# Kernel optimization log

Hardware: AMD Instinct MI355X
Metric: run time of the kernel (lower is better)

Reference implementation:

```python
import jax, jax.numpy as jnp
import numpy as np

B, D, S = 16384, 1024, 2048
LN_EPS = 1e-5


def setup_inputs() -> dict:
    key = jax.random.key(0)
    ks = jax.random.split(key, 16)
    inv_d = 1.0 / np.sqrt(D)
    inv_s = 1.0 / np.sqrt(S)
    inv_ds = 1.0 / np.sqrt(D + S)
    return {
        "x_t": jax.random.normal(ks[0], (B, D), jnp.float32),
        "state": jax.random.normal(ks[1], (B, S), jnp.float32),
        "conditioning": jax.random.normal(ks[2], (B, D), jnp.float32),
        "carry_scale": jax.random.uniform(ks[3], (B, S), jnp.float32),
        # Linear weights stored [in, out] (y = x @ W + b); equivalent math to torch's x @ W.T
        "W_step": jax.random.normal(ks[4], (D, S), jnp.float32) * inv_d,
        "b_step": jnp.zeros((S,), jnp.float32),
        "W_cstep": jax.random.normal(ks[5], (D, S), jnp.float32) * inv_d,
        "W_in": jax.random.normal(ks[6], (D, S), jnp.float32) * inv_d,
        "b_in": jnp.zeros((S,), jnp.float32),
        "W_cin": jax.random.normal(ks[7], (D, S), jnp.float32) * inv_d,
        "W_state": jax.random.normal(ks[8], (S, S), jnp.float32) * inv_s,
        "W_out": jax.random.normal(ks[9], (D + S, D), jnp.float32) * inv_ds,
        "b_out": jnp.zeros((D,), jnp.float32),
        "ln_w": jnp.ones((D,), jnp.float32),
        "ln_b": jnp.zeros((D,), jnp.float32),
        "log_decay": jnp.zeros((S,), jnp.float32),
    }


def reference(x_t, state, conditioning, carry_scale,
              W_step, b_step, W_cstep, W_in, b_in, W_cin,
              W_state, W_out, b_out, ln_w, ln_b, log_decay):
    # input-conditioned step size
    step = jax.nn.softplus(x_t @ W_step + b_step)
    step = step + 0.1 * jax.nn.softplus(conditioning @ W_cstep)
    # candidate state
    proposal = jnp.tanh(x_t @ W_in + b_in + conditioning @ W_cin + state @ W_state)
    # diagonal decay gate
    decay = jnp.exp(-step * jnp.exp(log_decay)) * carry_scale
    new_state = decay * state + (1.0 - decay) * proposal
    # output projection + residual LayerNorm
    out = jnp.concatenate([x_t, new_state], axis=-1) @ W_out + b_out
    h = out + x_t
    mu = jnp.mean(h, axis=-1, keepdims=True)
    var = jnp.mean(jnp.square(h - mu), axis=-1, keepdims=True)
    output = (h - mu) * jax.lax.rsqrt(var + LN_EPS) * ln_w + ln_b
    return output, new_state
```

## Files before the change

kernel.cpp:

```cpp
#include <hip/hip_runtime.h>
#include <hip/hip_bf16.h>
#include <cstdint>
#include <cstddef>

#define BB 16384
#define DD 1024
#define SS 2048

typedef __attribute__((ext_vector_type(8))) short s8vec;
typedef __attribute__((ext_vector_type(4))) short s4vec;
typedef __attribute__((ext_vector_type(4))) float f4vec;

static __device__ __forceinline__ short f2bf(float x) {
  __hip_bfloat16 h = __float2bfloat16(x);
  union { __hip_bfloat16 b; short s; } u; u.b = h; return u.s;
}

static __device__ __forceinline__ float softplus_f(float x) {
  return (x > 20.f) ? x : log1pf(expf(x));
}

static __device__ __forceinline__ void gload16(const void* g, void* l) {
  __builtin_amdgcn_global_load_lds((__attribute__((address_space(1))) void*)g,
                                   (__attribute__((address_space(3))) void*)l,
                                   16, 0, 0);
}

struct EpiParams {
  float* out;
  const float* bias;
  const float* step;
  const float* state;
  const float* carry;
  const float* ldec;
  float* out_state;
  short* xy;
  const float* x;
};

#define BAR() do { asm volatile("" ::: "memory"); __builtin_amdgcn_s_barrier(); asm volatile("" ::: "memory"); } while (0)
#define WAIT_LGKM0() do { asm volatile("s_waitcnt lgkmcnt(0)" ::: "memory"); __builtin_amdgcn_sched_barrier(0); } while (0)
#define WAIT_VM(n)   do { asm volatile("s_waitcnt vmcnt(" #n ")" ::: "memory"); __builtin_amdgcn_sched_barrier(0); } while (0)

template<int EPI>
__global__ __launch_bounds__(512, 2)
void gemm256(const short* __restrict__ A, int lda,
             const short* __restrict__ Bt, int ldb,
             int K, int nbxl, EpiParams ep)
{
  __shared__ short lds0[65536];

  const int tid  = threadIdx.x;
  const int lane = tid & 63;
  const int w    = tid >> 6;
  const int wm   = w >> 2;
  const int wn   = w & 3;
  const int frow = lane & 15;
  const int klane = lane >> 4;
  const int swb  = lane & 7;

  const int lin = blockIdx.x;
  const int bm  = lin >> nbxl;
  const int bn  = lin & ((1 << nbxl) - 1);

  const int rl0    = w * 16 + (lane >> 3);
  const int colsw8 = ((lane & 7) ^ ((lane >> 3) & 7)) * 8;
  const int dOff   = w * 1024 + lane * 8;

  const short* gA0 = A  + (size_t)(bm * 256 +       rl0) * lda + colsw8;
  const short* gA1 = A  + (size_t)(bm * 256 + 128 + rl0) * lda + colsw8;
  const short* gB0 = Bt + (size_t)(bn * 256 +       rl0) * ldb + colsw8;
  const short* gB1 = Bt + (size_t)(bn * 256 + 128 + rl0) * ldb + colsw8;
  const int kmax = K - 64;

  auto STAGE = [&](int buf, int h, int kt) {
    const short* g = (h == 0) ? gA0 : (h == 1) ? gA1 : (h == 2) ? gB0 : gB1;
    const int ld = (h < 2) ? lda : ldb;
    int kk = kt * 64; if (kk > kmax) kk = kmax;
    short* d = &lds0[buf * 32768 + h * 8192 + dOff];
    gload16(g + kk,                 d);
    gload16(g + kk + (size_t)8 * ld, d + 512);
  };

  auto LDA2 = [&](int buf, int frp, s8vec (&a)[2][2]) {
    const short* base = &lds0[buf * 32768 + wm * 8192];
#pragma unroll
    for (int i = 0; i < 2; i++) {
      const int row = (frp * 2 + i) * 16 + frow;
#pragma unroll
      for (int ks = 0; ks < 2; ks++) {
        const int slot = (ks * 4 + klane) ^ swb;
        a[i][ks] = *(const s8vec*)&base[row * 64 + slot * 8];
      }
    }
  };

  auto LDB8 = [&](int buf, s8vec (&b)[4][2]) {
    const short* base = &lds0[buf * 32768 + 16384 + (wn >> 1) * 8192];
#pragma unroll
    for (int fc = 0; fc < 4; fc++) {
      const int row = (wn & 1) * 64 + fc * 16 + frow;
#pragma unroll
      for (int ks = 0; ks < 2; ks++) {
        const int slot = (ks * 4 + klane) ^ swb;
        b[fc][ks] = *(const s8vec*)&base[row * 64 + slot * 8];
      }
    }
  };

  f4vec acc[8][4];
#pragma unroll
  for (int i = 0; i < 8; i++)
#pragma unroll
    for (int j = 0; j < 4; j++) acc[i][j] = (f4vec){0.f, 0.f, 0.f, 0.f};

  s8vec aX[2][2], aY[2][2], bf0[4][2], bf1[4][2];

#define QMFMA(aS, bS, q) do {                                                  \
  _Pragma("unroll") for (int i = 0; i < 2; i++)                                \
  _Pragma("unroll") for (int fc = 0; fc < 4; fc++)                             \
  _Pragma("unroll") for (int ks = 0; ks < 2; ks++)                             \
    acc[(q) * 2 + i][fc] = __builtin_amdgcn_mfma_f32_16x16x32_bf16(            \
        aS[i][ks], bS[fc][ks], acc[(q) * 2 + i][fc], 0, 0, 0);                 \
} while (0)

  STAGE(0, 0, 0); STAGE(0, 1, 0); STAGE(0, 2, 0); STAGE(0, 3, 0);
  STAGE(1, 0, 1);
  WAIT_VM(2);
  BAR();
  LDB8(0, bf0);
  LDA2(0, 0, aX);

  const int J = K >> 7;
  for (int j = 0; j < J; ++j) {
    const int t1 = 2 * j + 1, t2 = 2 * j + 2, t3 = 2 * j + 3;
    LDA2(0, 1, aY); STAGE(1, 1, t1);
    BAR(); WAIT_LGKM0();
    __builtin_amdgcn_s_setprio(1); QMFMA(aX, bf0, 0); __builtin_amdgcn_s_setprio(0);
    BAR();
    LDA2(0, 2, aX); STAGE(1, 2, t1);
    BAR(); WAIT_LGKM0();
    __builtin_amdgcn_s_setprio(1); QMFMA(aY, bf0, 1); __builtin_amdgcn_s_setprio(0);
    BAR();
    LDA2(0, 3, aY); STAGE(1, 3, t1);
    BAR(); WAIT_LGKM0();
    __builtin_amdgcn_s_setprio(1); QMFMA(aX, bf0, 2); __builtin_amdgcn_s_setprio(0);
    BAR();
    STAGE(0, 0, t2);
    WAIT_VM(2);
    BAR();
    LDB8(1, bf1); LDA2(1, 0, aX);
    __builtin_amdgcn_s_setprio(1); QMFMA(aY, bf0, 3); __builtin_amdgcn_s_setprio(0);
    BAR();
    LDA2(1, 1, aY); STAGE(0, 1, t2);
    BAR(); WAIT_LGKM0();
    __builtin_amdgcn_s_setprio(1); QMFMA(aX, bf1, 0); __builtin_amdgcn_s_setprio(0);
    BAR();
    LDA2(1, 2, aX); STAGE(0, 2, t2);
    BAR(); WAIT_LGKM0();
    __builtin_amdgcn_s_setprio(1); QMFMA(aY, bf1, 1); __builtin_amdgcn_s_setprio(0);
    BAR();
    LDA2(1, 3, aY); STAGE(0, 3, t2);
    BAR(); WAIT_LGKM0();
    __builtin_amdgcn_s_setprio(1); QMFMA(aX, bf1, 2); __builtin_amdgcn_s_setprio(0);
    BAR();
    STAGE(1, 0, t3);
    WAIT_VM(2);
    BAR();
    LDB8(0, bf0); LDA2(0, 0, aX);
    __builtin_amdgcn_s_setprio(1); QMFMA(aY, bf1, 3); __builtin_amdgcn_s_setprio(0);
    BAR();
  }
  asm volatile("s_waitcnt vmcnt(0) lgkmcnt(0)" ::: "memory");

  const int r0 = bm * 256 + wm * 128 + (lane >> 4) * 4;
  const int c0 = bn * 256 + wn * 64 + (lane & 15);

#pragma unroll
  for (int fr = 0; fr < 8; fr++) {
#pragma unroll
    for (int fc = 0; fc < 4; fc++) {
      const int col = c0 + fc * 16;
#pragma unroll
      for (int r = 0; r < 4; r++) {
        const int row = r0 + fr * 16 + r;
        const float v = acc[fr][fc][r];
        if constexpr (EPI == 0) {
          ep.out[(size_t)row * SS + col] = softplus_f(v + ep.bias[col]);
        } else if constexpr (EPI == 1) {
          const size_t idx = (size_t)row * SS + col;
          ep.out[idx] = ep.out[idx] + 0.1f * softplus_f(v);
        } else if constexpr (EPI == 2) {
          const size_t idx = (size_t)row * SS + col;
          const float step = ep.step[idx];
          const float dec  = expf(-step * expf(ep.ldec[col])) * ep.carry[idx];
          const float prop = tanhf(v + ep.bias[col]);
          const float ns   = dec * ep.state[idx] + (1.f - dec) * prop;
          ep.out_state[idx] = ns;
          ep.xy[(size_t)row * 3072 + 1024 + col] = f2bf(ns);
        } else {
          const size_t idx = (size_t)row * DD + col;
          ep.out[idx] = v + ep.bias[col] + ep.x[idx];
        }
      }
    }
  }
#undef QMFMA
}

__global__ __launch_bounds__(256)
void tcast(const float* __restrict__ src, int R, int C,
           short* __restrict__ dst, int ldd, int co)
{
  __shared__ float tile[32][33];
  const int c0 = blockIdx.x * 32;
  const int r0 = blockIdx.y * 32;
  const int tx = threadIdx.x;
  const int ty = threadIdx.y;
#pragma unroll
  for (int i = 0; i < 4; i++)
    tile[ty * 4 + i][tx] = src[(size_t)(r0 + ty * 4 + i) * C + c0 + tx];
  __syncthreads();
#pragma unroll
  for (int i = 0; i < 4; i++)
    dst[(size_t)(c0 + ty * 4 + i) * ldd + co + r0 + tx] = f2bf(tile[tx][ty * 4 + i]);
}

__global__ __launch_bounds__(256)
void cast_xc(const float4* __restrict__ x, const float4* __restrict__ c,
             short* __restrict__ Xcat, short* __restrict__ XY)
{
  const size_t i = (size_t)blockIdx.x * 256 + threadIdx.x;
  if (i >= (size_t)BB * (DD / 4)) return;
  const size_t row = i >> 8;
  const int col4 = (int)(i & 255);
  const float4 xv = x[i];
  const float4 cv = c[i];
  const s4vec xs = { f2bf(xv.x), f2bf(xv.y), f2bf(xv.z), f2bf(xv.w) };
  const s4vec cs = { f2bf(cv.x), f2bf(cv.y), f2bf(cv.z), f2bf(cv.w) };
  *(s4vec*)&Xcat[row * 4096 + col4 * 4]        = xs;
  *(s4vec*)&Xcat[row * 4096 + 1024 + col4 * 4] = cs;
  *(s4vec*)&XY[row * 3072 + col4 * 4]          = xs;
}

__global__ __launch_bounds__(256)
void cast_state(const float4* __restrict__ s, short* __restrict__ Xcat)
{
  const size_t i = (size_t)blockIdx.x * 256 + threadIdx.x;
  if (i >= (size_t)BB * (SS / 4)) return;
  const size_t row = i >> 9;
  const int col4 = (int)(i & 511);
  const float4 sv = s[i];
  const s4vec ss = { f2bf(sv.x), f2bf(sv.y), f2bf(sv.z), f2bf(sv.w) };
  *(s4vec*)&Xcat[row * 4096 + 2048 + col4 * 4] = ss;
}

__global__ __launch_bounds__(256)
void ln_kernel(const float* __restrict__ h, const float* __restrict__ w,
               const float* __restrict__ b, float* __restrict__ out)
{
  const int row = blockIdx.x;
  const int t = threadIdx.x;
  const float4 v = ((const float4*)(h + (size_t)row * DD))[t];
  float s  = v.x + v.y + v.z + v.w;
  float sq = v.x * v.x + v.y * v.y + v.z * v.z + v.w * v.w;
#pragma unroll
  for (int off = 32; off; off >>= 1) {
    s  += __shfl_down(s, off);
    sq += __shfl_down(sq, off);
  }
  __shared__ float ss[4], ssq[4];
  const int lane = t & 63, wv = t >> 6;
  if (lane == 0) { ss[wv] = s; ssq[wv] = sq; }
  __syncthreads();
  const float st  = ss[0] + ss[1] + ss[2] + ss[3];
  const float sqt = ssq[0] + ssq[1] + ssq[2] + ssq[3];
  const float mu  = st * (1.f / (float)DD);
  const float var = sqt * (1.f / (float)DD) - mu * mu;
  const float rstd = rsqrtf(var + 1e-5f);
  const float4 wv4 = ((const float4*)w)[t];
  const float4 bv4 = ((const float4*)b)[t];
  float4 o;
  o.x = (v.x - mu) * rstd * wv4.x + bv4.x;
  o.y = (v.y - mu) * rstd * wv4.y + bv4.y;
  o.z = (v.z - mu) * rstd * wv4.z + bv4.z;
  o.w = (v.w - mu) * rstd * wv4.w + bv4.w;
  ((float4*)(out + (size_t)row * DD))[t] = o;
}

extern "C" void kernel_launch(void* const* d_in, const int* in_sizes, int n_in,
                              void* d_out, int out_size, void* d_ws, size_t ws_size,
                              hipStream_t stream)
{
  const float* x_t    = (const float*)d_in[0];
  const float* state  = (const float*)d_in[1];
  const float* cond   = (const float*)d_in[2];
  const float* carry  = (const float*)d_in[3];
  const float* W_step = (const float*)d_in[4];
  const float* b_step = (const float*)d_in[5];
  const float* W_cstep= (const float*)d_in[6];
  const float* W_in   = (const float*)d_in[7];
  const float* b_in   = (const float*)d_in[8];
  const float* W_cin  = (const float*)d_in[9];
  const float* W_state= (const float*)d_in[10];
  const float* W_out  = (const float*)d_in[11];
  const float* b_out  = (const float*)d_in[12];
  const float* ln_w   = (const float*)d_in[13];
  const float* ln_b   = (const float*)d_in[14];
  const float* ldec   = (const float*)d_in[15];

  char* ws = (char*)d_ws;
  size_t off = 0;
  short* Xcat = (short*)(ws + off); off += (size_t)BB * 4096 * 2;
  short* XY   = (short*)(ws + off); off += (size_t)BB * 3072 * 2;
  float* A1   = (float*)(ws + off); off += (size_t)BB * SS * 4;
  short* WstepT  = (short*)(ws + off); off += (size_t)SS * DD * 2;
  short* WcstepT = (short*)(ws + off); off += (size_t)SS * DD * 2;
  short* WcatT   = (short*)(ws + off); off += (size_t)SS * 4096 * 2;
  short* WoutT   = (short*)(ws + off); off += (size_t)DD * 3072 * 2;
  float* hbuf = A1;

  float* out_ln    = (float*)d_out;
  float* out_state = (float*)d_out + (size_t)BB * DD;

  cast_xc<<<dim3(BB * (DD / 4) / 256), 256, 0, stream>>>(
      (const float4*)x_t, (const float4*)cond, Xcat, XY);
  cast_state<<<dim3(BB * (SS / 4) / 256), 256, 0, stream>>>(
      (const float4*)state, Xcat);

  tcast<<<dim3(SS / 32, DD / 32), dim3(32, 8), 0, stream>>>(W_step, DD, SS, WstepT, DD, 0);
  tcast<<<dim3(SS / 32, DD / 32), dim3(32, 8), 0, stream>>>(W_cstep, DD, SS, WcstepT, DD, 0);
  tcast<<<dim3(SS / 32, DD / 32), dim3(32, 8), 0, stream>>>(W_in,   DD, SS, WcatT, 4096, 0);
  tcast<<<dim3(SS / 32, DD / 32), dim3(32, 8), 0, stream>>>(W_cin,  DD, SS, WcatT, 4096, 1024);
  tcast<<<dim3(SS / 32, SS / 32), dim3(32, 8), 0, stream>>>(W_state, SS, SS, WcatT, 4096, 2048);
  tcast<<<dim3(DD / 32, 3072 / 32), dim3(32, 8), 0, stream>>>(W_out, 3072, DD, WoutT, 3072, 0);

  const int nwgS = (BB / 256) * (SS / 256);
  const int nwgD = (BB / 256) * (DD / 256);

  EpiParams p1{}; p1.out = A1; p1.bias = b_step;
  gemm256<0><<<dim3(nwgS), 512, 0, stream>>>(Xcat, 4096, WstepT, DD, 1024, 3, p1);

  EpiParams p2{}; p2.out = A1;
  gemm256<1><<<dim3(nwgS), 512, 0, stream>>>(Xcat + 1024, 4096, WcstepT, DD, 1024, 3, p2);

  EpiParams p3{};
  p3.bias = b_in; p3.step = A1; p3.state = state; p3.carry = carry;
  p3.ldec = ldec; p3.out_state = out_state; p3.xy = XY;
  gemm256<2><<<dim3(nwgS), 512, 0, stream>>>(Xcat, 4096, WcatT, 4096, 4096, 3, p3);

  EpiParams p4{}; p4.out = hbuf; p4.bias = b_out; p4.x = x_t;
  gemm256<3><<<dim3(nwgD), 512, 0, stream>>>(XY, 3072, WoutT, 3072, 3072, 2, p4);

  ln_kernel<<<dim3(BB), 256, 0, stream>>>(hbuf, ln_w, ln_b, out_ln);
}
```

Baseline: 1.576 ms.

## Restructure GEMM main loop to full-tile fragment loads and remap blocks per XCD

The GEMM main loop now loads all A and B fragments for a K-tile into registers at once, rather than interleaving small A loads with MFMA quarters. It issues the next tile's global-to-LDS stages between MFMA groups and uses fewer barriers per iteration. A block-index remap also assigns contiguous output tiles to each of the 8 XCDs, which is meant to improve L2 reuse. The cost is more live fragment registers, which could spill or lower occupancy, plus a different balance between load latency hiding and compute.

```diff
diff --git a/kernel.cpp b/kernel.cpp
--- a/kernel.cpp
+++ b/kernel.cpp
@@ -46,7 +46,7 @@
 __global__ __launch_bounds__(512, 2)
 void gemm256(const short* __restrict__ A, int lda,
              const short* __restrict__ Bt, int ldb,
-             int K, int nbxl, EpiParams ep)
+             int K, int nbxl, int qchunk, EpiParams ep)
 {
   __shared__ short lds0[65536];
 
@@ -59,9 +59,10 @@
   const int klane = lane >> 4;
   const int swb  = lane & 7;
 
-  const int lin = blockIdx.x;
-  const int bm  = lin >> nbxl;
-  const int bn  = lin & ((1 << nbxl) - 1);
+  const int lin  = blockIdx.x;
+  const int orig = (lin & 7) * qchunk + (lin >> 3);
+  const int bm   = orig >> nbxl;
+  const int bn   = orig & ((1 << nbxl) - 1);
 
   const int rl0    = w * 16 + (lane >> 3);
   const int colsw8 = ((lane & 7) ^ ((lane >> 3) & 7)) * 8;
@@ -78,97 +79,75 @@
     const int ld = (h < 2) ? lda : ldb;
     int kk = kt * 64; if (kk > kmax) kk = kmax;
     short* d = &lds0[buf * 32768 + h * 8192 + dOff];
-    gload16(g + kk,                 d);
+    gload16(g + kk,                  d);
     gload16(g + kk + (size_t)8 * ld, d + 512);
   };
 
-  auto LDA2 = [&](int buf, int frp, s8vec (&a)[2][2]) {
-    const short* base = &lds0[buf * 32768 + wm * 8192];
-#pragma unroll
-    for (int i = 0; i < 2; i++) {
-      const int row = (frp * 2 + i) * 16 + frow;
-#pragma unroll
-      for (int ks = 0; ks < 2; ks++) {
-        const int slot = (ks * 4 + klane) ^ swb;
-        a[i][ks] = *(const s8vec*)&base[row * 64 + slot * 8];
-      }
+  s8vec aF[8][2];
+  s8vec bF[4][2];
+
+  auto LDALL = [&](int buf) {
+    const short* bB = &lds0[buf * 32768 + 16384 + (wn >> 1) * 8192];
+#pragma unroll
+    for (int fc = 0; fc < 4; fc++) {
+      const int row = (wn & 1) * 64 + fc * 16 + frow;
+#pragma unroll
+      for (int ks = 0; ks < 2; ks++)
+        bF[fc][ks] = *(const s8vec*)&bB[row * 64 + ((ks * 4 + klane) ^ swb) * 8];
+    }
+    const short* bA = &lds0[buf * 32768 + wm * 8192];
+#pragma unroll
+    for (int fr = 0; fr < 8; fr++) {
+      const int row = fr * 16 + frow;
+#pragma unroll
+      for (int ks = 0; ks < 2; ks++)
+        aF[fr][ks] = *(const s8vec*)&bA[row * 64 + ((ks * 4 + klane) ^ swb) * 8];
     }
   };
 
-  auto LDB8 = [&](int buf, s8vec (&b)[4][2]) {
-    const short* base = &lds0[buf * 32768 + 16384 + (wn >> 1) * 8192];
-#pragma unroll
-    for (int fc = 0; fc < 4; fc++) {
-      const int row = (wn & 1) * 64 + fc * 16 + frow;
-#pragma unroll
-      for (int ks = 0; ks < 2; ks++) {
-        const int slot = (ks * 4 + klane) ^ swb;
-        b[fc][ks] = *(const s8vec*)&base[row * 64 + slot * 8];
-      }
-    }
-  };
-
   f4vec acc[8][4];
 #pragma unroll
   for (int i = 0; i < 8; i++)
 #pragma unroll
     for (int j = 0; j < 4; j++) acc[i][j] = (f4vec){0.f, 0.f, 0.f, 0.f};
 
-  s8vec aX[2][2], aY[2][2], bf0[4][2], bf1[4][2];
-
-#define QMFMA(aS, bS, q) do {                                                  \
+#define QMFMA(q) do {                                                          \
+  __builtin_amdgcn_s_setprio(1);                                              \
   _Pragma("unroll") for (int i = 0; i < 2; i++)                                \
   _Pragma("unroll") for (int fc = 0; fc < 4; fc++)                             \
   _Pragma("unroll") for (int ks = 0; ks < 2; ks++)                             \
     acc[(q) * 2 + i][fc] = __builtin_amdgcn_mfma_f32_16x16x32_bf16(            \
-        aS[i][ks], bS[fc][ks], acc[(q) * 2 + i][fc], 0, 0, 0);                 \
+        aF[(q) * 2 + i][ks], bF[fc][ks], acc[(q) * 2 + i][fc], 0, 0, 0);       \
+  __builtin_amdgcn_s_setprio(0);                                              \
 } while (0)
 
   STAGE(0, 0, 0); STAGE(0, 1, 0); STAGE(0, 2, 0); STAGE(0, 3, 0);
-  STAGE(1, 0, 1);
-  WAIT_VM(2);
+  STAGE(1, 0, 1); STAGE(1, 1, 1); STAGE(1, 2, 1); STAGE(1, 3, 1);
+  WAIT_VM(8);
   BAR();
-  LDB8(0, bf0);
-  LDA2(0, 0, aX);
 
   const int J = K >> 7;
   for (int j = 0; j < J; ++j) {
-    const int t1 = 2 * j + 1, t2 = 2 * j + 2, t3 = 2 * j + 3;
-    LDA2(0, 1, aY); STAGE(1, 1, t1);
-    BAR(); WAIT_LGKM0();
-    __builtin_amdgcn_s_setprio(1); QMFMA(aX, bf0, 0); __builtin_amdgcn_s_setprio(0);
+    const int t2 = 2 * j + 2, t3 = 2 * j + 3;
+    LDALL(0);
+    QMFMA(0);
+    WAIT_LGKM0(); BAR();
+    STAGE(0, 0, t2); STAGE(0, 1, t2);
+    QMFMA(1);
+    STAGE(0, 2, t2); STAGE(0, 3, t2);
+    QMFMA(2);
+    QMFMA(3);
+    WAIT_VM(8);
     BAR();
-    LDA2(0, 2, aX); STAGE(1, 2, t1);
-    BAR(); WAIT_LGKM0();
-    __builtin_amdgcn_s_setprio(1); QMFMA(aY, bf0, 1); __builtin_amdgcn_s_setprio(0);
-    BAR();
-    LDA2(0, 3, aY); STAGE(1, 3, t1);
-    BAR(); WAIT_LGKM0();
-    __builtin_amdgcn_s_setprio(1); QMFMA(aX, bf0, 2); __builtin_amdgcn_s_setprio(0);
-    BAR();
-    STAGE(0, 0, t2);
-    WAIT_VM(2);
-    BAR();
-    LDB8(1, bf1); LDA2(1, 0, aX);
-    __builtin_amdgcn_s_setprio(1); QMFMA(aY, bf0, 3); __builtin_amdgcn_s_setprio(0);
-    BAR();
-    LDA2(1, 1, aY); STAGE(0, 1, t2);
-    BAR(); WAIT_LGKM0();
-    __builtin_amdgcn_s_setprio(1); QMFMA(aX, bf1, 0); __builtin_amdgcn_s_setprio(0);
-    BAR();
-    LDA2(1, 2, aX); STAGE(0, 2, t2);
-    BAR(); WAIT_LGKM0();
-    __builtin_amdgcn_s_setprio(1); QMFMA(aY, bf1, 1); __builtin_amdgcn_s_setprio(0);
-    BAR();
-    LDA2(1, 3, aY); STAGE(0, 3, t2);
-    BAR(); WAIT_LGKM0();
-    __builtin_amdgcn_s_setprio(1); QMFMA(aX, bf1, 2); __builtin_amdgcn_s_setprio(0);
-    BAR();
-    STAGE(1, 0, t3);
-    WAIT_VM(2);
-    BAR();
-    LDB8(0, bf0); LDA2(0, 0, aX);
-    __builtin_amdgcn_s_setprio(1); QMFMA(aY, bf1, 3); __builtin_amdgcn_s_setprio(0);
+    LDALL(1);
+    QMFMA(0);
+    WAIT_LGKM0(); BAR();
+    STAGE(1, 0, t3); STAGE(1, 1, t3);
+    QMFMA(1);
+    STAGE(1, 2, t3); STAGE(1, 3, t3);
+    QMFMA(2);
+    QMFMA(3);
+    WAIT_VM(8);
     BAR();
   }
   asm volatile("s_waitcnt vmcnt(0) lgkmcnt(0)" ::: "memory");
@@ -339,18 +318,18 @@
   const int nwgD = (BB / 256) * (DD / 256);
 
   EpiParams p1{}; p1.out = A1; p1.bias = b_step;
-  gemm256<0><<<dim3(nwgS), 512, 0, stream>>>(Xcat, 4096, WstepT, DD, 1024, 3, p1);
+  gemm256<0><<<dim3(nwgS), 512, 0, stream>>>(Xcat, 4096, WstepT, DD, 1024, 3, nwgS / 8, p1);
 
   EpiParams p2{}; p2.out = A1;
-  gemm256<1><<<dim3(nwgS), 512, 0, stream>>>(Xcat + 1024, 4096, WcstepT, DD, 1024, 3, p2);
+  gemm256<1><<<dim3(nwgS), 512, 0, stream>>>(Xcat + 1024, 4096, WcstepT, DD, 1024, 3, nwgS / 8, p2);
 
   EpiParams p3{};
   p3.bias = b_in; p3.step = A1; p3.state = state; p3.carry = carry;
   p3.ldec = ldec; p3.out_state = out_state; p3.xy = XY;
-  gemm256<2><<<dim3(nwgS), 512, 0, stream>>>(Xcat, 4096, WcatT, 4096, 4096, 3, p3);
+  gemm256<2><<<dim3(nwgS), 512, 0, stream>>>(Xcat, 4096, WcatT, 4096, 4096, 3, nwgS / 8, p3);
 
   EpiParams p4{}; p4.out = hbuf; p4.bias = b_out; p4.x = x_t;
-  gemm256<3><<<dim3(nwgD), 512, 0, stream>>>(XY, 3072, WoutT, 3072, 3072, 2, p4);
+  gemm256<3><<<dim3(nwgD), 512, 0, stream>>>(XY, 3072, WoutT, 3072, 3072, 2, nwgD / 8, p4);
 
   ln_kernel<<<dim3(BB), 256, 0, stream>>>(hbuf, ln_w, ln_b, out_ln);
 }
```

Result: slower. 2.095 ms (+33.0%).
